# Performance work log

Measured on AMD Instinct MI355X. Metric: run time of the kernel, lower is better.

Reference implementation:

```python
import jax, jax.numpy as jnp
import numpy as np

IN_DIMS = 4
DEPTH = 4
C = IN_DIMS + 1                     # channels after time augmentation
SIG = sum(C ** k for k in range(1, DEPTH + 1))  # 780
N, T = 64, 1024


def setup_inputs() -> dict:
    key = jax.random.key(0)
    k1, k2, k3, k4, k5 = jax.random.split(key, 5)
    batch = jax.random.normal(k1, (N, T, IN_DIMS), dtype=jnp.float32)
    s_c = 1.0 / np.sqrt(C)
    conv_w = jax.random.normal(k2, (C, C), dtype=jnp.float32) * s_c
    conv_b = jax.random.normal(k3, (C,), dtype=jnp.float32) * s_c
    s_l = 1.0 / np.sqrt(SIG)
    lin_w = jax.random.normal(k4, (SIG, SIG), dtype=jnp.float32) * s_l
    lin_b = jax.random.normal(k5, (SIG,), dtype=jnp.float32) * s_l
    return {"batch": batch, "conv_w": conv_w, "conv_b": conv_b,
            "lin_w": lin_w, "lin_b": lin_b}


def _stream_signature(path):
    """Streamed path signature with zero basepoint.

    path: (n, t, C). Returns (n, t, SIG) where entry t is the signature of
    the piecewise-linear path (0, path[0], ..., path[t]) truncated at DEPTH,
    levels flattened in lexicographic (row-major) order like signatory.
    """
    n = path.shape[0]
    # increments; basepoint=True means first increment is path[:,0] - 0
    dx = jnp.concatenate([path[:, :1, :], path[:, 1:, :] - path[:, :-1, :]], axis=1)
    init = tuple(jnp.zeros((n, C ** k), path.dtype) for k in range(1, DEPTH + 1))

    def step(levels, d):
        # exp(d) in the truncated tensor algebra: e_k = d^{(x)k} / k!
        e = [d]
        for k in range(2, DEPTH + 1):
            e.append((jnp.einsum('na,nb->nab', e[-1], d) / k).reshape(n, -1))
        # Chen: new_k = e_k + S_k + sum_{i=1}^{k-1} S_i (x) e_{k-i}
        new = []
        for k in range(1, DEPTH + 1):
            acc = levels[k - 1] + e[k - 1]
            for i in range(1, k):
                acc = acc + jnp.einsum('na,nb->nab', levels[i - 1], e[k - i - 1]).reshape(n, -1)
            new.append(acc)
        new = tuple(new)
        return new, jnp.concatenate(new, axis=-1)

    _, ys = jax.lax.scan(step, init, jnp.swapaxes(dx, 0, 1))  # ys: (t, n, SIG)
    return jnp.swapaxes(ys, 0, 1)


def reference(batch, conv_w, conv_b, lin_w, lin_b):
    n, t, _ = batch.shape
    # time augmentation: append channel arange(1,T+1)/T
    time = (jnp.arange(1, t + 1, dtype=batch.dtype) / t)[None, :, None]
    a = jnp.concatenate([batch, jnp.broadcast_to(time, (n, t, 1))], axis=-1)  # (n,t,C)
    # kernel-size-1 conv1d == pointwise linear over channels
    b = a @ conv_w.T + conv_b                                                  # (n,t,C)
    c = _stream_signature(b)                                                   # (n,t,SIG)
    # zero out the first stream entry (torch.concat of zeros with c[:,1:,:])
    c = jnp.concatenate([jnp.zeros((n, 1, SIG), c.dtype), c[:, 1:, :]], axis=1)
    return jnp.tanh(c @ lin_w.T + lin_b)
```

## Files before the change

kernel.cpp:

```cpp
#include <hip/hip_runtime.h>
#include <math.h>

#define N_B 64
#define T_LEN 1024
#define IN_D 4
#define CH 5
#define SIG 780
#define KP 800
#define SEG_LEN 16
#define N_SEG 64
#define SC_L1 1.0f
#define SC_L2 0.25f
#define SC_L3 0.0625f
#define SC_L4 0.015625f

typedef _Float16 f16x8 __attribute__((ext_vector_type(8)));
typedef float f32x4 __attribute__((ext_vector_type(4)));

typedef __attribute__((address_space(1))) const void* as1cp;
typedef __attribute__((address_space(3))) void* as3p;

#define VMCNT(n) asm volatile("s_waitcnt vmcnt(" #n ")" ::: "memory")

__device__ __forceinline__ float fast_tanh(float x) {
  float ax = fabsf(x);
  float e = __expf(-2.0f * ax);
  float r = (1.0f - e) * __builtin_amdgcn_rcpf(1.0f + e);
  return copysignf(r, x);
}

__global__ __launch_bounds__(256) void conv_kernel(
    const float* __restrict__ batch,
    const float* __restrict__ conv_w,
    const float* __restrict__ conv_b,
    float* __restrict__ b_out) {
  int idx = blockIdx.x * blockDim.x + threadIdx.x;
  if (idx >= N_B * T_LEN) return;
  int t = idx & (T_LEN - 1);
  const float* a = batch + (size_t)idx * IN_D;
  float a0 = a[0], a1 = a[1], a2 = a[2], a3 = a[3];
  float tm = (float)(t + 1) / (float)T_LEN;
  float* o = b_out + (size_t)idx * CH;
#pragma unroll
  for (int j = 0; j < CH; ++j) {
    const float* w = conv_w + j * CH;
    float r = conv_b[j];
    r = fmaf(tm, w[4], r);
    r = fmaf(a3, w[3], r);
    r = fmaf(a2, w[2], r);
    r = fmaf(a1, w[1], r);
    r = fmaf(a0, w[0], r);
    o[j] = r;
  }
}

__global__ __launch_bounds__(320) void seg_kernel(
    const float* __restrict__ batch,
    const float* __restrict__ conv_w,
    const float* __restrict__ conv_b,
    float* __restrict__ P) {
  int s = blockIdx.x;
  int n = blockIdx.y;
  int tid = threadIdx.x;

  __shared__ float S[2][SIG];
  __shared__ float bc[(SEG_LEN + 1) * CH];
  __shared__ float dsh[SEG_LEN][CH];

  for (int i = tid; i < SIG; i += 320) S[0][i] = 0.0f;
  if (tid < (SEG_LEN + 1) * CH) {
    int r = s * SEG_LEN - 1 + tid / CH, ch = tid % CH;
    float v = 0.0f;
    if (r >= 0) {
      const float* a = batch + ((size_t)n * T_LEN + r) * IN_D;
      const float* w = conv_w + ch * CH;
      v = conv_b[ch];
      v = fmaf(a[0], w[0], v);
      v = fmaf(a[1], w[1], v);
      v = fmaf(a[2], w[2], v);
      v = fmaf(a[3], w[3], v);
      v = fmaf((float)(r + 1) * (1.0f / T_LEN), w[4], v);
    }
    bc[tid] = v;
  }
  __syncthreads();
  if (tid < SEG_LEN * CH) {
    int j = tid / CH, ch = tid % CH;
    dsh[j][ch] = bc[(j + 1) * CH + ch] - bc[j * CH + ch];
  }

  const int x0 = tid;
  const int x1 = tid + 320;
  const bool has1 = (tid < 305);
  const int a0i = x0 / 125, b0i = (x0 / 25) % 5, c0i = (x0 / 5) % 5, d0i = x0 % 5;
  const int a1i = x1 / 125, b1i = (x1 / 25) % 5, c1i = (x1 / 5) % 5, d1i = x1 % 5;
  const int s2_0 = x0 / 25, s3_0 = x0 / 5;
  const int s2_1 = x1 / 25, s3_1 = x1 / 5;
  const bool hasL3 = (tid < 125);
  const int ya = tid / 25, yb = (tid / 5) % 5, yc = tid % 5;
  const bool hasL2 = (tid < 25);
  const int za = tid / 5, zb = tid % 5;
  const bool hasL1 = (tid < CH);
  __syncthreads();

  int c = 0;
  for (int j = 0; j < SEG_LEN; ++j) {
    const float* Sc = S[c];
    float* Sn = S[c ^ 1];
    float n4_0, n4_1 = 0.0f, n3 = 0.0f, n2 = 0.0f, n1 = 0.0f;
    {
      float tH = fmaf(0.25f, dsh[j][a0i], Sc[a0i]);
      tH = fmaf((1.0f / 3.0f) * dsh[j][b0i], tH, Sc[5 + s2_0]);
      tH = fmaf(0.5f * dsh[j][c0i], tH, Sc[30 + s3_0]);
      n4_0 = fmaf(dsh[j][d0i], tH, Sc[155 + x0]);
    }
    if (has1) {
      float tH = fmaf(0.25f, dsh[j][a1i], Sc[a1i]);
      tH = fmaf((1.0f / 3.0f) * dsh[j][b1i], tH, Sc[5 + s2_1]);
      tH = fmaf(0.5f * dsh[j][c1i], tH, Sc[30 + s3_1]);
      n4_1 = fmaf(dsh[j][d1i], tH, Sc[155 + x1]);
    }
    if (hasL3) {
      float tH = fmaf((1.0f / 3.0f), dsh[j][ya], Sc[ya]);
      tH = fmaf(0.5f * dsh[j][yb], tH, Sc[5 + ya * 5 + yb]);
      n3 = fmaf(dsh[j][yc], tH, Sc[30 + tid]);
    }
    if (hasL2) {
      float tH = fmaf(0.5f, dsh[j][za], Sc[za]);
      n2 = fmaf(dsh[j][zb], tH, Sc[5 + tid]);
    }
    if (hasL1) n1 = Sc[tid] + dsh[j][tid];
    Sn[155 + x0] = n4_0;
    if (has1) Sn[155 + x1] = n4_1;
    if (hasL3) Sn[30 + tid] = n3;
    if (hasL2) Sn[5 + tid] = n2;
    if (hasL1) Sn[tid] = n1;
    __syncthreads();
    c ^= 1;
  }

  float* Pr = P + ((size_t)n * N_SEG + s) * SIG;
  for (int i = tid; i < SIG; i += 320) Pr[i] = S[c][i];
}

__global__ __launch_bounds__(640) void prefix_kernel(float* __restrict__ P) {
  int n = blockIdx.x;
  int tid = threadIdx.x;
  __shared__ float A[2][SIG];
  __shared__ float Bs[SIG];

  float* Pn = P + (size_t)n * N_SEG * SIG;
  for (int i = tid; i < SIG; i += 640) A[0][i] = Pn[i];
  int i0 = tid, i1 = tid + 640;
  float r0 = 0.f, r1 = 0.f;
  if (i0 < SIG) r0 = Pn[SIG + i0];
  if (i1 < SIG) r1 = Pn[SIG + i1];

  const int e4 = tid;
  const int q4a = e4 / 125, r125 = e4 % 125, r25 = e4 % 25, r5 = e4 % 5;
  const int e4d5 = e4 / 5, e4d25 = e4 / 25;
  const int e3 = tid;
  const int e3a = e3 / 25, e3r25 = e3 % 25, e3r5 = e3 % 5, e3d5 = e3 / 5;
  const int e2 = tid - 125;
  const int e1 = tid - 150;

  int c = 0;
  for (int s = 1; s < N_SEG; ++s) {
    if (i0 < SIG) Bs[i0] = r0;
    if (i1 < SIG) Bs[i1] = r1;
    __syncthreads();
    if (s + 1 < N_SEG) {
      const float* Pnx = Pn + (size_t)(s + 1) * SIG;
      if (i0 < SIG) r0 = Pnx[i0];
      if (i1 < SIG) r1 = Pnx[i1];
    }
    const float* Ac = A[c];
    float* An = A[c ^ 1];
    float* Po = Pn + (size_t)s * SIG;
    if (tid < 625) {
      float v4 = Ac[155 + e4] + Bs[155 + e4];
      v4 = fmaf(Ac[30 + e4d5], Bs[r5], v4);
      v4 = fmaf(Ac[5 + e4d25], Bs[5 + r25], v4);
      v4 = fmaf(Ac[q4a], Bs[30 + r125], v4);
      An[155 + e4] = v4; Po[155 + e4] = v4;
    }
    if (tid < 125) {
      float v3 = Ac[30 + e3] + Bs[30 + e3];
      v3 = fmaf(Ac[5 + e3d5], Bs[e3r5], v3);
      v3 = fmaf(Ac[e3a], Bs[5 + e3r25], v3);
      An[30 + e3] = v3; Po[30 + e3] = v3;
    } else if (tid < 150) {
      float v2 = Ac[5 + e2] + Bs[5 + e2];
      v2 = fmaf(Ac[e2 / 5], Bs[e2 % 5], v2);
      An[5 + e2] = v2; Po[5 + e2] = v2;
    } else if (tid < 155) {
      float v1 = Ac[e1] + Bs[e1];
      An[e1] = v1; Po[e1] = v1;
    }
    c ^= 1;
  }
}

__global__ __launch_bounds__(320) void emit_kernel(
    const float* __restrict__ batch,
    const float* __restrict__ conv_w,
    const float* __restrict__ conv_b,
    const float* __restrict__ P,
    _Float16* __restrict__ c1,
    _Float16* __restrict__ c2) {
  int s = blockIdx.x;
  int n = blockIdx.y;
  int tid = threadIdx.x;

  __shared__ float S[2][SIG];
  __shared__ float bc[(SEG_LEN + 1) * CH];
  __shared__ float dsh[SEG_LEN][CH];
  __shared__ __align__(16) _Float16 row1[2][KP];
  __shared__ __align__(16) _Float16 row2[2][KP];

  if (s == 0) {
    for (int i = tid; i < SIG; i += 320) S[0][i] = 0.0f;
  } else {
    const float* Pr = P + ((size_t)n * N_SEG + (s - 1)) * SIG;
    for (int i = tid; i < SIG; i += 320) S[0][i] = Pr[i];
  }
  if (tid < (SEG_LEN + 1) * CH) {
    int r = s * SEG_LEN - 1 + tid / CH, ch = tid % CH;
    float v = 0.0f;
    if (r >= 0) {
      const float* a = batch + ((size_t)n * T_LEN + r) * IN_D;
      const float* w = conv_w + ch * CH;
      v = conv_b[ch];
      v = fmaf(a[0], w[0], v);
      v = fmaf(a[1], w[1], v);
      v = fmaf(a[2], w[2], v);
      v = fmaf(a[3], w[3], v);
      v = fmaf((float)(r + 1) * (1.0f / T_LEN), w[4], v);
    }
    bc[tid] = v;
  }
  if (tid < KP - SIG) {
    row1[0][SIG + tid] = (_Float16)0.0f;
    row1[1][SIG + tid] = (_Float16)0.0f;
    row2[0][SIG + tid] = (_Float16)0.0f;
    row2[1][SIG + tid] = (_Float16)0.0f;
  }
  __syncthreads();
  if (tid < SEG_LEN * CH) {
    int j = tid / CH, ch = tid % CH;
    dsh[j][ch] = bc[(j + 1) * CH + ch] - bc[j * CH + ch];
  }

  const int x0 = tid;
  const int x1 = tid + 320;
  const bool has1 = (tid < 305);
  const int a0i = x0 / 125, b0i = (x0 / 25) % 5, c0i = (x0 / 5) % 5, d0i = x0 % 5;
  const int a1i = x1 / 125, b1i = (x1 / 25) % 5, c1i = (x1 / 5) % 5, d1i = x1 % 5;
  const int s2_0 = x0 / 25, s3_0 = x0 / 5;
  const int s2_1 = x1 / 25, s3_1 = x1 / 5;
  const bool hasL3 = (tid < 125);
  const int ya = tid / 25, yb = (tid / 5) % 5, yc = tid % 5;
  const bool hasL2 = (tid < 25);
  const int za = tid / 5, zb = tid % 5;
  const bool hasL1 = (tid < CH);
  __syncthreads();

  int c = 0;
  for (int j = 0; j < SEG_LEN; ++j) {
    int t = s * SEG_LEN + j;
    const float* Sc = S[c];
    float* Sn = S[c ^ 1];
    float n4_0, n4_1 = 0.0f, n3 = 0.0f, n2 = 0.0f, n1 = 0.0f;
    {
      float tH = fmaf(0.25f, dsh[j][a0i], Sc[a0i]);
      tH = fmaf((1.0f / 3.0f) * dsh[j][b0i], tH, Sc[5 + s2_0]);
      tH = fmaf(0.5f * dsh[j][c0i], tH, Sc[30 + s3_0]);
      n4_0 = fmaf(dsh[j][d0i], tH, Sc[155 + x0]);
    }
    if (has1) {
      float tH = fmaf(0.25f, dsh[j][a1i], Sc[a1i]);
      tH = fmaf((1.0f / 3.0f) * dsh[j][b1i], tH, Sc[5 + s2_1]);
      tH = fmaf(0.5f * dsh[j][c1i], tH, Sc[30 + s3_1]);
      n4_1 = fmaf(dsh[j][d1i], tH, Sc[155 + x1]);
    }
    if (hasL3) {
      float tH = fmaf((1.0f / 3.0f), dsh[j][ya], Sc[ya]);
      tH = fmaf(0.5f * dsh[j][yb], tH, Sc[5 + ya * 5 + yb]);
      n3 = fmaf(dsh[j][yc], tH, Sc[30 + tid]);
    }
    if (hasL2) {
      float tH = fmaf(0.5f, dsh[j][za], Sc[za]);
      n2 = fmaf(dsh[j][zb], tH, Sc[5 + tid]);
    }
    if (hasL1) n1 = Sc[tid] + dsh[j][tid];

    if (j > 0) {
      size_t base = ((size_t)n * T_LEN + (t - 1)) * KP;
      if (tid < 100) {
        *(float4*)(c1 + base + tid * 8) = *(const float4*)&row1[c][tid * 8];
      } else if (tid < 200) {
        int cc = tid - 100;
        *(float4*)(c2 + base + cc * 8) = *(const float4*)&row2[c][cc * 8];
      }
    }

    Sn[155 + x0] = n4_0;
    if (has1) Sn[155 + x1] = n4_1;
    if (hasL3) Sn[30 + tid] = n3;
    if (hasL2) Sn[5 + tid] = n2;
    if (hasL1) Sn[tid] = n1;

    float z = (t == 0) ? 0.0f : 1.0f;
    {
      float v = n4_0 * SC_L4 * z;
      _Float16 h = (_Float16)v;
      row1[c ^ 1][155 + x0] = h; row2[c ^ 1][155 + x0] = (_Float16)(v - (float)h);
    }
    if (has1) {
      float v = n4_1 * SC_L4 * z;
      _Float16 h = (_Float16)v;
      row1[c ^ 1][155 + x1] = h; row2[c ^ 1][155 + x1] = (_Float16)(v - (float)h);
    }
    if (hasL3) {
      float v = n3 * SC_L3 * z;
      _Float16 h = (_Float16)v;
      row1[c ^ 1][30 + tid] = h; row2[c ^ 1][30 + tid] = (_Float16)(v - (float)h);
    }
    if (hasL2) {
      float v = n2 * SC_L2 * z;
      _Float16 h = (_Float16)v;
      row1[c ^ 1][5 + tid] = h; row2[c ^ 1][5 + tid] = (_Float16)(v - (float)h);
    }
    if (hasL1) {
      float v = n1 * SC_L1 * z;
      _Float16 h = (_Float16)v;
      row1[c ^ 1][tid] = h; row2[c ^ 1][tid] = (_Float16)(v - (float)h);
    }
    __syncthreads();
    c ^= 1;
  }
  {
    size_t base = ((size_t)n * T_LEN + (s * SEG_LEN + SEG_LEN - 1)) * KP;
    if (tid < 100) {
      *(float4*)(c1 + base + tid * 8) = *(const float4*)&row1[c][tid * 8];
    } else if (tid < 200) {
      int cc = tid - 100;
      *(float4*)(c2 + base + cc * 8) = *(const float4*)&row2[c][cc * 8];
    }
  }
}

__global__ __launch_bounds__(256) void wconv_kernel(
    const float* __restrict__ W,
    _Float16* __restrict__ w1,
    _Float16* __restrict__ w2) {
  int idx = blockIdx.x * blockDim.x + threadIdx.x;
  if (idx >= 896 * KP) return;
  int nn = idx / KP, k = idx % KP;
  float v = 0.0f;
  if (nn < SIG && k < SIG) {
    float sc = (k < 5) ? 1.0f : (k < 30) ? 4.0f : (k < 155) ? 16.0f : 64.0f;
    v = W[(size_t)nn * SIG + k] * sc;
  }
  _Float16 h = (_Float16)v;
  w1[idx] = h;
  w2[idx] = (_Float16)(v - (float)h);
}

__global__ __launch_bounds__(512, 2) void gemm_mfma(
    const _Float16* __restrict__ A1p, const _Float16* __restrict__ A2p,
    const _Float16* __restrict__ B1p, const _Float16* __restrict__ B2p,
    const float* __restrict__ bias, float* __restrict__ out) {
  __shared__ _Float16 Al[3][2][256 * 32];
  __shared__ _Float16 Bl[3][2][128 * 32];

  int tid = threadIdx.x;
  int lane = tid & 63, wid = tid >> 6;
  int wm = wid >> 1, wn = wid & 1;

  int b = blockIdx.x;
  int xcd = b & 7, sidx = b >> 3;
  int mt = (sidx / 7) * 8 + xcd;
  int nt = sidx % 7;
  int m0 = mt * 256;
  int n0 = nt * 128;

  f32x4 acc[4][4];
#pragma unroll
  for (int i = 0; i < 4; ++i)
#pragma unroll
    for (int j = 0; j < 4; ++j) acc[i][j] = (f32x4){0.f, 0.f, 0.f, 0.f};

  int sr = lane >> 2, scn = lane & 3;
  int swst = (sr ^ (sr >> 2)) & 3;
  int qg = scn ^ swst;
  int fr = lane & 15, fq = lane >> 4;
  int swf = (fr ^ (fr >> 2)) & 3;
  int fchunk = fq ^ swf;

  auto stageA = [&](int kb, int buf, int i) {
    int k0 = kb * 32;
    int linear = wid * 4 + i;
    int plane = linear >> 4, grp = linear & 15;
    size_t g = (size_t)(m0 + grp * 16 + sr) * KP + k0 + qg * 8;
    const _Float16* src = (plane ? A2p : A1p) + g;
    __builtin_amdgcn_global_load_lds((as1cp)src, (as3p)(&Al[buf][plane][grp * 512]), 16, 0, 0);
  };
  auto stageB = [&](int kb, int buf, int i) {
    int k0 = kb * 32;
    int linear = wid * 2 + i;
    int plane = linear >> 3, grp = linear & 7;
    size_t g = (size_t)(n0 + grp * 16 + sr) * KP + k0 + qg * 8;
    const _Float16* src = (plane ? B2p : B1p) + g;
    __builtin_amdgcn_global_load_lds((as1cp)src, (as3p)(&Bl[buf][plane][grp * 512]), 16, 0, 0);
  };

#pragma unroll
  for (int i = 0; i < 4; ++i) stageA(0, 0, i);
#pragma unroll
  for (int i = 0; i < 2; ++i) stageB(0, 0, i);
#pragma unroll
  for (int i = 0; i < 4; ++i) stageA(1, 1, i);
#pragma unroll
  for (int i = 0; i < 2; ++i) stageB(1, 1, i);

  int cur = 0;
#pragma unroll 1
  for (int kb = 0; kb < 25; ++kb) {
    int nx = cur + 2; if (nx >= 3) nx -= 3;
    bool pf = (kb + 2 < 25);
    if (kb < 24) { VMCNT(6); } else { VMCNT(0); }
    __builtin_amdgcn_s_barrier();
    __builtin_amdgcn_sched_barrier(0);
    f16x8 a1f[4], a2f[4], b1f[4], b2f[4];
    {
      int off = (wn * 64 + 0 * 16 + fr) * 32 + fchunk * 8;
      b1f[0] = *(const f16x8*)&Bl[cur][0][off];
      b2f[0] = *(const f16x8*)&Bl[cur][1][off];
    }
#pragma unroll
    for (int tm = 0; tm < 4; ++tm) {
      int off = (wm * 64 + tm * 16 + fr) * 32 + fchunk * 8;
      a1f[tm] = *(const f16x8*)&Al[cur][0][off];
      a2f[tm] = *(const f16x8*)&Al[cur][1][off];
    }
#pragma unroll
    for (int tn = 1; tn < 4; ++tn) {
      int off = (wn * 64 + tn * 16 + fr) * 32 + fchunk * 8;
      b1f[tn] = *(const f16x8*)&Bl[cur][0][off];
      b2f[tn] = *(const f16x8*)&Bl[cur][1][off];
    }
    if (pf) {
      stageA(kb + 2, nx, 0); stageA(kb + 2, nx, 1);
      stageA(kb + 2, nx, 2); stageA(kb + 2, nx, 3);
      stageB(kb + 2, nx, 0); stageB(kb + 2, nx, 1);
    }
    __builtin_amdgcn_s_setprio(1);
#pragma unroll
    for (int tn = 0; tn < 4; ++tn) {
#pragma unroll
      for (int tm = 0; tm < 4; ++tm) {
        acc[tm][tn] = __builtin_amdgcn_mfma_f32_16x16x32_f16(a1f[tm], b1f[tn], acc[tm][tn], 0, 0, 0);
        acc[tm][tn] = __builtin_amdgcn_mfma_f32_16x16x32_f16(a1f[tm], b2f[tn], acc[tm][tn], 0, 0, 0);
        acc[tm][tn] = __builtin_amdgcn_mfma_f32_16x16x32_f16(a2f[tm], b1f[tn], acc[tm][tn], 0, 0, 0);
      }
    }
    __builtin_amdgcn_s_setprio(0);
    cur = cur + 1; if (cur >= 3) cur -= 3;
  }
  __syncthreads();

  float* ep = (float*)(&Al[0][0][0]) + wid * 2112;

  float bv[4];
#pragma unroll
  for (int tn = 0; tn < 4; ++tn) {
    int nn = n0 + wn * 64 + tn * 16 + fr;
    bv[tn] = (nn < SIG) ? bias[nn] : 0.0f;
  }
#pragma unroll
  for (int h = 0; h < 2; ++h) {
#pragma unroll
    for (int tm2 = 0; tm2 < 2; ++tm2) {
      int tm = h * 2 + tm2;
#pragma unroll
      for (int tn = 0; tn < 4; ++tn) {
#pragma unroll
        for (int r = 0; r < 4; ++r) {
          int lr = tm2 * 16 + fq * 4 + r;
          int lc = tn * 16 + fr;
          ep[lr * 66 + lc] = fast_tanh(acc[tm][tn][r] + bv[tn]);
        }
      }
    }
#pragma unroll
    for (int p = 0; p < 2; ++p) {
      int lr = lane & 31;
      int ck = (lane >> 5) * 2 + p;
      int gm = m0 + wm * 64 + h * 32 + lr;
      int gc0 = n0 + wn * 64 + ck * 16;
#pragma unroll
      for (int q = 0; q < 4; ++q) {
        int col = gc0 + q * 4;
        if (col + 3 < SIG) {
          *(float4*)(out + (size_t)gm * SIG + col) =
              *(const float4*)&ep[lr * 66 + ck * 16 + q * 4];
        } else if (col < SIG) {
#pragma unroll
          for (int e = 0; e < 4; ++e) {
            int c2 = col + e;
            if (c2 < SIG) out[(size_t)gm * SIG + c2] = ep[lr * 66 + ck * 16 + q * 4 + e];
          }
        }
      }
    }
  }
}

__global__ __launch_bounds__(320) void sig_kernel_fb(
    const float* __restrict__ b_in, float* __restrict__ c_out) {
  int n = blockIdx.x;
  int tid = threadIdx.x;
  __shared__ float S[SIG];
  __shared__ float bc[64 * CH];
  __shared__ float dsh[CH];
  __shared__ float pb[CH];
  for (int i = tid; i < SIG; i += 320) S[i] = 0.0f;
  if (tid < CH) pb[tid] = 0.0f;
  const float* bn = b_in + (size_t)n * T_LEN * CH;
  float* cn = c_out + (size_t)n * T_LEN * SIG;
  const int x0 = tid, x1 = tid + 320;
  const bool has1 = (tid < 305);
  const int a0i = x0 / 125, b0i = (x0 / 25) % 5, c0i = (x0 / 5) % 5, d0i = x0 % 5;
  const int a1i = x1 / 125, b1i = (x1 / 25) % 5, c1i = (x1 / 5) % 5, d1i = x1 % 5;
  const int s2_0 = x0 / 25, s3_0 = x0 / 5, s2_1 = x1 / 25, s3_1 = x1 / 5;
  const bool hasL3 = (tid < 125);
  const int ya = tid / 25, yb = (tid / 5) % 5, yc = tid % 5;
  const bool hasL2 = (tid < 25);
  const int za = tid / 5, zb = tid % 5;
  const bool hasL1 = (tid < CH);
  for (int t = 0; t < T_LEN; ++t) {
    if ((t & 63) == 0) {
      __syncthreads();
      bc[tid] = bn[t * CH + tid];
      __syncthreads();
    }
    if (tid < CH) {
      float cur = bc[(t & 63) * CH + tid];
      dsh[tid] = cur - pb[tid];
      pb[tid] = cur;
    }
    __syncthreads();
    float n4_0, n4_1 = 0.0f, n3 = 0.0f, n2 = 0.0f, n1 = 0.0f;
    {
      float tH = fmaf(0.25f, dsh[a0i], S[a0i]);
      tH = fmaf((1.0f / 3.0f) * dsh[b0i], tH, S[5 + s2_0]);
      tH = fmaf(0.5f * dsh[c0i], tH, S[30 + s3_0]);
      n4_0 = fmaf(dsh[d0i], tH, S[155 + x0]);
    }
    if (has1) {
      float tH = fmaf(0.25f, dsh[a1i], S[a1i]);
      tH = fmaf((1.0f / 3.0f) * dsh[b1i], tH, S[5 + s2_1]);
      tH = fmaf(0.5f * dsh[c1i], tH, S[30 + s3_1]);
      n4_1 = fmaf(dsh[d1i], tH, S[155 + x1]);
    }
    if (hasL3) {
      float tH = fmaf((1.0f / 3.0f), dsh[ya], S[ya]);
      tH = fmaf(0.5f * dsh[yb], tH, S[5 + ya * 5 + yb]);
      n3 = fmaf(dsh[yc], tH, S[30 + tid]);
    }
    if (hasL2) {
      float tH = fmaf(0.5f, dsh[za], S[za]);
      n2 = fmaf(dsh[zb], tH, S[5 + tid]);
    }
    if (hasL1) n1 = S[tid] + dsh[tid];
    __syncthreads();
    S[155 + x0] = n4_0;
    if (has1) S[155 + x1] = n4_1;
    if (hasL3) S[30 + tid] = n3;
    if (hasL2) S[5 + tid] = n2;
    if (hasL1) S[tid] = n1;
    float* crow = cn + (size_t)t * SIG;
    float z = (t == 0) ? 0.0f : 1.0f;
    crow[155 + x0] = n4_0 * z;
    if (has1) crow[155 + x1] = n4_1 * z;
    if (hasL3) crow[30 + tid] = n3 * z;
    if (hasL2) crow[5 + tid] = n2 * z;
    if (hasL1) crow[tid] = n1 * z;
    __syncthreads();
  }
}

#define BM 256
#define BN 64
#define BK 16
__global__ __launch_bounds__(256) void gemm_tanh_fb(
    const float* __restrict__ Cmat, const float* __restrict__ W,
    const float* __restrict__ bias, float* __restrict__ out) {
  __shared__ float As[BK][BM + 4];
  __shared__ float Ws[BK][BN + 4];
  int tid = threadIdx.x;
  int tx = tid & 7, ty = tid >> 3;
  int m0 = blockIdx.x * BM, n0 = blockIdx.y * BN;
  float acc[8][8];
#pragma unroll
  for (int i = 0; i < 8; ++i)
#pragma unroll
    for (int j = 0; j < 8; ++j) acc[i][j] = 0.0f;
  for (int kb = 0; kb < SIG; kb += BK) {
    __syncthreads();
#pragma unroll
    for (int p = 0; p < 4; ++p) {
      int id = tid + p * 256;
      int row = id >> 2, kg = (id & 3) * 4, gk = kb + kg;
      float4 v = make_float4(0.f, 0.f, 0.f, 0.f);
      if (gk < SIG) v = *(const float4*)(Cmat + (size_t)(m0 + row) * SIG + gk);
      As[kg + 0][row] = v.x; As[kg + 1][row] = v.y;
      As[kg + 2][row] = v.z; As[kg + 3][row] = v.w;
    }
    {
      int row = tid >> 2, kg = (tid & 3) * 4, gk = kb + kg, wr = n0 + row;
      float4 v = make_float4(0.f, 0.f, 0.f, 0.f);
      if (gk < SIG && wr < SIG) v = *(const float4*)(W + (size_t)wr * SIG + gk);
      Ws[kg + 0][row] = v.x; Ws[kg + 1][row] = v.y;
      Ws[kg + 2][row] = v.z; Ws[kg + 3][row] = v.w;
    }
    __syncthreads();
#pragma unroll
    for (int k = 0; k < BK; ++k) {
      float af[8], wf[8];
      *(float4*)&af[0] = *(const float4*)&As[k][ty * 8];
      *(float4*)&af[4] = *(const float4*)&As[k][ty * 8 + 4];
      *(float4*)&wf[0] = *(const float4*)&Ws[k][tx * 8];
      *(float4*)&wf[4] = *(const float4*)&Ws[k][tx * 8 + 4];
#pragma unroll
      for (int i = 0; i < 8; ++i)
#pragma unroll
        for (int j = 0; j < 8; ++j) acc[i][j] = fmaf(af[i], wf[j], acc[i][j]);
    }
  }
#pragma unroll
  for (int i = 0; i < 8; ++i) {
    int m = m0 + ty * 8 + i;
    float* orow = out + (size_t)m * SIG;
#pragma unroll
    for (int jj = 0; jj < 8; jj += 4) {
      int col = n0 + tx * 8 + jj;
      if (col < SIG) {
        float4 r;
        r.x = tanhf(acc[i][jj + 0] + bias[col + 0]);
        r.y = tanhf(acc[i][jj + 1] + bias[col + 1]);
        r.z = tanhf(acc[i][jj + 2] + bias[col + 2]);
        r.w = tanhf(acc[i][jj + 3] + bias[col + 3]);
        *(float4*)(orow + col) = r;
      }
    }
  }
}

extern "C" void kernel_launch(void* const* d_in, const int* in_sizes, int n_in,
                              void* d_out, int out_size, void* d_ws, size_t ws_size,
                              hipStream_t stream) {
  const float* batch = (const float*)d_in[0];
  const float* conv_w = (const float*)d_in[1];
  const float* conv_b = (const float*)d_in[2];
  const float* lin_w = (const float*)d_in[3];
  const float* lin_b = (const float*)d_in[4];
  float* out = (float*)d_out;

  const size_t plane_elems = (size_t)N_B * T_LEN * KP;
  const size_t wplane_elems = (size_t)896 * KP;
  const size_t P_elems = (size_t)N_B * N_SEG * SIG;
  const size_t bp_elems = (size_t)N_B * T_LEN * CH;
  const size_t need_big = 2 * plane_elems * sizeof(_Float16) +
                          2 * wplane_elems * sizeof(_Float16) +
                          P_elems * sizeof(float);

  if (ws_size >= need_big) {
    _Float16* c1 = (_Float16*)d_ws;
    _Float16* c2 = c1 + plane_elems;
    _Float16* w1 = c2 + plane_elems;
    _Float16* w2 = w1 + wplane_elems;
    float* P = (float*)(w2 + wplane_elems);

    wconv_kernel<<<dim3((896 * KP + 255) / 256), dim3(256), 0, stream>>>(
        lin_w, w1, w2);
    seg_kernel<<<dim3(N_SEG, N_B), dim3(320), 0, stream>>>(batch, conv_w, conv_b, P);
    prefix_kernel<<<dim3(N_B), dim3(640), 0, stream>>>(P);
    emit_kernel<<<dim3(N_SEG, N_B), dim3(320), 0, stream>>>(
        batch, conv_w, conv_b, P, c1, c2);
    gemm_mfma<<<dim3(1792), dim3(512), 0, stream>>>(c1, c2, w1, w2, lin_b, out);
  } else {
    float* b_path = (float*)d_ws;
    float* c_sig = (float*)d_ws + bp_elems;
    conv_kernel<<<dim3((N_B * T_LEN + 255) / 256), dim3(256), 0, stream>>>(
        batch, conv_w, conv_b, b_path);
    sig_kernel_fb<<<dim3(N_B), dim3(320), 0, stream>>>(b_path, c_sig);
    gemm_tanh_fb<<<dim3((N_B * T_LEN) / BM, (SIG + BN - 1) / BN), dim3(256), 0, stream>>>(
        c_sig, lin_w, lin_b, out);
  }
}
```

Before: 624.3 us.

## Double-buffer MFMA fragments in registers to overlap LDS reads with MFMAs

Restructures the GEMM main loop so the LDS fragment reads for block k+1 go into a second register set while the MFMAs for block k run from the first set. The loop is unrolled by two to alternate the register sets, and the prologue and epilogue are adjusted to match. The global-to-LDS prefetch is now issued before the barrier, and the wait also covers lgkmcnt, so LDS-read latency is hidden behind matrix math instead of stalling it. The cost is twice as many fragment registers, which raises VGPR pressure and could lower occupancy or cause spills.

```diff
diff --git a/kernel.cpp b/kernel.cpp
--- a/kernel.cpp
+++ b/kernel.cpp
@@ -415,6 +415,34 @@
     __builtin_amdgcn_global_load_lds((as1cp)src, (as3p)(&Bl[buf][plane][grp * 512]), 16, 0, 0);
   };
 
+  f16x8 xa1[4], xa2[4], xb1[4], xb2[4];
+  f16x8 ya1[4], ya2[4], yb1[4], yb2[4];
+
+#define READF(A1v, A2v, B1v, B2v, rbuf)                              \
+  {                                                                  \
+    _Pragma("unroll") for (int tm = 0; tm < 4; ++tm) {               \
+      int off = (wm * 64 + tm * 16 + fr) * 32 + fchunk * 8;          \
+      A1v[tm] = *(const f16x8*)&Al[rbuf][0][off];                    \
+      A2v[tm] = *(const f16x8*)&Al[rbuf][1][off];                    \
+    }                                                                \
+    _Pragma("unroll") for (int tn = 0; tn < 4; ++tn) {               \
+      int off = (wn * 64 + tn * 16 + fr) * 32 + fchunk * 8;          \
+      B1v[tn] = *(const f16x8*)&Bl[rbuf][0][off];                    \
+      B2v[tn] = *(const f16x8*)&Bl[rbuf][1][off];                    \
+    }                                                                \
+  }
+
+#define MFMAS(A1v, A2v, B1v, B2v)                                                                     \
+  __builtin_amdgcn_s_setprio(1);                                                                      \
+  _Pragma("unroll") for (int tn = 0; tn < 4; ++tn) {                                                  \
+    _Pragma("unroll") for (int tm = 0; tm < 4; ++tm) {                                                \
+      acc[tm][tn] = __builtin_amdgcn_mfma_f32_16x16x32_f16(A1v[tm], B1v[tn], acc[tm][tn], 0, 0, 0);   \
+      acc[tm][tn] = __builtin_amdgcn_mfma_f32_16x16x32_f16(A1v[tm], B2v[tn], acc[tm][tn], 0, 0, 0);   \
+      acc[tm][tn] = __builtin_amdgcn_mfma_f32_16x16x32_f16(A2v[tm], B1v[tn], acc[tm][tn], 0, 0, 0);   \
+    }                                                                                                 \
+  }                                                                                                   \
+  __builtin_amdgcn_s_setprio(0);
+
 #pragma unroll
   for (int i = 0; i < 4; ++i) stageA(0, 0, i);
 #pragma unroll
@@ -423,51 +451,42 @@
   for (int i = 0; i < 4; ++i) stageA(1, 1, i);
 #pragma unroll
   for (int i = 0; i < 2; ++i) stageB(1, 1, i);
-
-  int cur = 0;
+  VMCNT(6);
+  __builtin_amdgcn_s_barrier();
+  __builtin_amdgcn_sched_barrier(0);
+  READF(xa1, xa2, xb1, xb2, 0);
+
+  int rb = 1, sb = 2;
+#define BODY(kb, CA1, CA2, CB1, CB2, NA1, NA2, NB1, NB2)             \
+  {                                                                  \
+    if ((kb) + 2 < 25) {                                             \
+      stageA((kb) + 2, sb, 0); stageA((kb) + 2, sb, 1);              \
+      stageA((kb) + 2, sb, 2); stageA((kb) + 2, sb, 3);              \
+      stageB((kb) + 2, sb, 0); stageB((kb) + 2, sb, 1);              \
+      asm volatile("s_waitcnt vmcnt(6) lgkmcnt(0)" ::: "memory");    \
+    } else {                                                         \
+      asm volatile("s_waitcnt vmcnt(0) lgkmcnt(0)" ::: "memory");    \
+    }                                                                \
+    __builtin_amdgcn_s_barrier();                                    \
+    __builtin_amdgcn_sched_barrier(0);                               \
+    READF(NA1, NA2, NB1, NB2, rb);                                   \
+    __builtin_amdgcn_sched_barrier(0);                               \
+    MFMAS(CA1, CA2, CB1, CB2);                                       \
+    rb = rb + 1; if (rb == 3) rb = 0;                                \
+    sb = sb + 1; if (sb == 3) sb = 0;                                \
+  }
+
 #pragma unroll 1
-  for (int kb = 0; kb < 25; ++kb) {
-    int nx = cur + 2; if (nx >= 3) nx -= 3;
-    bool pf = (kb + 2 < 25);
-    if (kb < 24) { VMCNT(6); } else { VMCNT(0); }
-    __builtin_amdgcn_s_barrier();
-    __builtin_amdgcn_sched_barrier(0);
-    f16x8 a1f[4], a2f[4], b1f[4], b2f[4];
-    {
-      int off = (wn * 64 + 0 * 16 + fr) * 32 + fchunk * 8;
-      b1f[0] = *(const f16x8*)&Bl[cur][0][off];
-      b2f[0] = *(const f16x8*)&Bl[cur][1][off];
-    }
-#pragma unroll
-    for (int tm = 0; tm < 4; ++tm) {
-      int off = (wm * 64 + tm * 16 + fr) * 32 + fchunk * 8;
-      a1f[tm] = *(const f16x8*)&Al[cur][0][off];
-      a2f[tm] = *(const f16x8*)&Al[cur][1][off];
-    }
-#pragma unroll
-    for (int tn = 1; tn < 4; ++tn) {
-      int off = (wn * 64 + tn * 16 + fr) * 32 + fchunk * 8;
-      b1f[tn] = *(const f16x8*)&Bl[cur][0][off];
-      b2f[tn] = *(const f16x8*)&Bl[cur][1][off];
-    }
-    if (pf) {
-      stageA(kb + 2, nx, 0); stageA(kb + 2, nx, 1);
-      stageA(kb + 2, nx, 2); stageA(kb + 2, nx, 3);
-      stageB(kb + 2, nx, 0); stageB(kb + 2, nx, 1);
-    }
-    __builtin_amdgcn_s_setprio(1);
-#pragma unroll
-    for (int tn = 0; tn < 4; ++tn) {
-#pragma unroll
-      for (int tm = 0; tm < 4; ++tm) {
-        acc[tm][tn] = __builtin_amdgcn_mfma_f32_16x16x32_f16(a1f[tm], b1f[tn], acc[tm][tn], 0, 0, 0);
-        acc[tm][tn] = __builtin_amdgcn_mfma_f32_16x16x32_f16(a1f[tm], b2f[tn], acc[tm][tn], 0, 0, 0);
-        acc[tm][tn] = __builtin_amdgcn_mfma_f32_16x16x32_f16(a2f[tm], b1f[tn], acc[tm][tn], 0, 0, 0);
-      }
-    }
-    __builtin_amdgcn_s_setprio(0);
-    cur = cur + 1; if (cur >= 3) cur -= 3;
-  }
+  for (int kk = 0; kk < 12; ++kk) {
+    int k0 = kk * 2;
+    BODY(k0,     xa1, xa2, xb1, xb2, ya1, ya2, yb1, yb2);
+    BODY(k0 + 1, ya1, ya2, yb1, yb2, xa1, xa2, xb1, xb2);
+  }
+  MFMAS(xa1, xa2, xb1, xb2);
+#undef BODY
+#undef READF
+#undef MFMAS
+
   __syncthreads();
 
   float* ep = (float*)(&Al[0][0][0]) + wid * 2112;
```

Measured after the change: 623.2 us. About the same (-0.2%).
